# Kernel optimization log

Hardware: AMD Instinct MI355X
Metric: run time of the kernel (lower is better)

Reference implementation:

```python
import jax, jax.numpy as jnp
import numpy as np
import math

EMBED_DIM = 768
NUM_HEADS = 12
SEQ_LEN = 2048
NUM_BLOCKS = 8
BLOCK_SIZE = EMBED_DIM // NUM_BLOCKS  # 96
HEAD_DIM = EMBED_DIM // NUM_HEADS     # 64
BATCH = 4


def build_sparse_mask(T):
    # local window of 5 (j in [i-4, i]) plus log-stride links at i-8, i-16, ...
    m = np.full((T, T), -np.inf, dtype=np.float32)
    for i in range(T):
        for j in range(max(0, i - 4), i + 1):
            m[i, j] = 0.0
        step = 8
        while i - step >= 0:
            m[i, i - step] = 0.0
            step *= 2
    return jnp.asarray(m)


def make_urdhva_params(key):
    k1, k2, k3 = jax.random.split(key, 3)
    s = BLOCK_SIZE ** 0.5
    Wv = jax.random.normal(k1, (NUM_BLOCKS, BLOCK_SIZE, BLOCK_SIZE), jnp.float32) / s
    Wr = jax.random.normal(k2, (NUM_BLOCKS - 1, BLOCK_SIZE, BLOCK_SIZE), jnp.float32) / s
    Wl = jax.random.normal(k3, (NUM_BLOCKS - 1, BLOCK_SIZE, BLOCK_SIZE), jnp.float32) / s
    b = jnp.zeros((EMBED_DIM,), jnp.float32)
    return Wv, Wr, Wl, b


def urdhva_linear(x, Wv, Wr, Wl, b):
    # x: [..., EMBED_DIM] -> block-diagonal + neighbor cross-block linear
    shp = x.shape
    xb = x.reshape(-1, NUM_BLOCKS, BLOCK_SIZE)  # [N, B, S]
    y = jnp.einsum('nbs,bst->nbt', xb, Wv)
    y = y.at[:, 1:, :].add(jnp.einsum('nbs,bst->nbt', xb[:, :-1, :], Wr))
    y = y.at[:, :-1, :].add(jnp.einsum('nbs,bst->nbt', xb[:, 1:, :], Wl))
    return y.reshape(shp) + b


def setup_inputs() -> dict:
    key = jax.random.key(0)
    kx, kq, kk, kv, ko = jax.random.split(key, 5)
    inp = {'x': jax.random.normal(kx, (BATCH, SEQ_LEN, EMBED_DIM), jnp.float32)}
    for name, k in (('q', kq), ('k', kk), ('v', kv), ('o', ko)):
        Wv, Wr, Wl, b = make_urdhva_params(k)
        inp[name + '_Wv'] = Wv
        inp[name + '_Wr'] = Wr
        inp[name + '_Wl'] = Wl
        inp[name + '_b'] = b
    inp['sparse_mask'] = build_sparse_mask(SEQ_LEN)
    return inp


def reference(x, q_Wv, q_Wr, q_Wl, q_b, k_Wv, k_Wr, k_Wl, k_b,
              v_Wv, v_Wr, v_Wl, v_b, o_Wv, o_Wr, o_Wl, o_b, sparse_mask):
    B, T, C = x.shape
    H, D = NUM_HEADS, HEAD_DIM
    q = urdhva_linear(x, q_Wv, q_Wr, q_Wl, q_b).reshape(B, T, H, D).transpose(0, 2, 1, 3)
    k = urdhva_linear(x, k_Wv, k_Wr, k_Wl, k_b).reshape(B, T, H, D).transpose(0, 2, 1, 3)
    v = urdhva_linear(x, v_Wv, v_Wr, v_Wl, v_b).reshape(B, T, H, D).transpose(0, 2, 1, 3)
    scores = jnp.einsum('bhqd,bhkd->bhqk', q, k) / math.sqrt(D)
    scores = scores + sparse_mask[:T, :T]
    attn = jax.nn.softmax(scores, axis=-1)
    out = jnp.einsum('bhqk,bhkd->bhqd', attn, v).transpose(0, 2, 1, 3).reshape(B, T, C)
    return urdhva_linear(out, o_Wv, o_Wr, o_Wl, o_b)
```

## Files before the change

kernel.cpp:

```cpp
#include <hip/hip_runtime.h>
#include <hip/hip_bf16.h>

typedef __hip_bfloat16 bf16;
typedef __attribute__((ext_vector_type(8))) short short8;
typedef __attribute__((ext_vector_type(4))) float f32x4;

#define ED 768
#define NB 8
#define BS 96
#define NH 12
#define HD 64
#define SEQ 2048
#define NBATCH 4
#define NROWS (NBATCH*SEQ)

__device__ __forceinline__ float b2f(bf16 v){ return __bfloat162float(v); }
__device__ __forceinline__ bf16 f2b(float v){ return __float2bfloat16(v); }
__device__ __forceinline__ short f2bs(float v){
    return (short)__builtin_bit_cast(unsigned short, __float2bfloat16(v));
}
__device__ __forceinline__ unsigned pkbf16(float lo, float hi){
    return (unsigned)(unsigned short)f2bs(lo) |
           ((unsigned)(unsigned short)f2bs(hi) << 16);
}
__device__ __forceinline__ void gload_lds16(const void* g, void* l) {
    __builtin_amdgcn_global_load_lds(
        (const __attribute__((address_space(1))) unsigned*)g,
        (__attribute__((address_space(3))) unsigned*)l, 16, 0, 0);
}

__global__ __launch_bounds__(256) void densify_t(
    const float* __restrict__ qWv, const float* __restrict__ qWr, const float* __restrict__ qWl,
    const float* __restrict__ kWv, const float* __restrict__ kWr, const float* __restrict__ kWl,
    const float* __restrict__ vWv, const float* __restrict__ vWr, const float* __restrict__ vWl,
    const float* __restrict__ oWv, const float* __restrict__ oWr, const float* __restrict__ oWl,
    bf16* __restrict__ WdBase)
{
    __shared__ __align__(16) bf16 tile[96][104];

    const int z = blockIdx.y;
    const float* Wv = (z==0)?qWv:(z==1)?kWv:(z==2)?vWv:oWv;
    const float* Wr = (z==0)?qWr:(z==1)?kWr:(z==2)?vWr:oWr;
    const float* Wl = (z==0)?qWl:(z==1)?kWl:(z==2)?vWl:oWl;
    bf16* Wd = WdBase + (size_t)z*ED*ED;

    const int m = blockIdx.x;
    const float* src; int bt, bs;
    if (m < 8)       { src = Wv + m*96*96;      bt = m;    bs = m;    }
    else if (m < 15) { src = Wr + (m-8)*96*96;  bt = m-7;  bs = m-8;  }
    else             { src = Wl + (m-15)*96*96; bt = m-15; bs = m-14; }

    const int tid = threadIdx.x;
    for (int i = tid; i < 96*96; i += 256) {
        const int ss = i / 96, tt = i - ss*96;
        tile[tt][ss] = f2b(src[i]);
    }
    __syncthreads();
    for (int i = tid; i < 96*12; i += 256) {
        const int tt = i / 12, s8 = (i - tt*12) << 3;
        *(short8*)(Wd + (size_t)(bt*96+tt)*ED + bs*96 + s8) =
            *(const short8*)&tile[tt][s8];
    }
    if (m < 8) {
        const int lo   = (bt == 0) ? 0 : (bt-1)*96;
        const int hi0  = (bt >= 7) ? ED : (bt+2)*96;
        const int zlo8 = lo >> 3;
        const int ztot = zlo8 + ((ED - hi0) >> 3);
        const short8 zz = (short8){0,0,0,0,0,0,0,0};
        for (int i = tid; i < 96*ztot; i += 256) {
            const int tt = i / ztot, q = i - tt*ztot;
            const int col8 = (q < zlo8) ? (q << 3) : (hi0 + ((q - zlo8) << 3));
            *(short8*)(Wd + (size_t)(bt*96+tt)*ED + col8) = zz;
        }
    }
}

__global__ __launch_bounds__(256, 2) void qkv_gemm_fused(
    const float* __restrict__ x,
    const bf16* __restrict__ WdBase,
    const float* __restrict__ qb, const float* __restrict__ kb,
    const float* __restrict__ vb,
    bf16* __restrict__ qo, bf16* __restrict__ ko, bf16* __restrict__ vT)
{
    __shared__ __align__(16) bf16 As[2][128*32];
    __shared__ __align__(16) bf16 Bs[2][3*96*32];

    const int tid  = threadIdx.x;
    const int lane = tid & 63;
    const int wave = tid >> 6;
    const int rowbase = blockIdx.x*128;
    const int ob = blockIdx.y;
    const int colbase = ob*BS;
    const int klo = (ob==0)    ? 0  : (ob-1)*BS;
    const int khi = (ob==NB-1) ? ED : (ob+2)*BS;
    const int nt  = (khi - klo) >> 5;

    const int ar  = tid >> 1;
    const int ah  = tid & 1;
    const int asw = ((ar & 15) ^ ((ar & 15) >> 2)) & 3;
    const int as0 = ((2*ah)   ^ asw) << 4;
    const int as1 = ((2*ah+1) ^ asw) << 4;
    const float* axbase = x + (size_t)(rowbase + ar)*ED + 16*ah;

    const int sub  = lane >> 2;
    const int slot = lane & 3;
    const int sws  = (sub ^ (sub >> 2)) & 3;
    const int kofs = ((slot ^ sws) << 3);

    f32x4 acc[3][2][6];
    #pragma unroll
    for (int z=0;z<3;++z)
        #pragma unroll
        for (int i=0;i<2;++i)
            #pragma unroll
            for (int j=0;j<6;++j) acc[z][i][j] = (f32x4){0.f,0.f,0.f,0.f};

    float4 fr0, fr1, fr2, fr3;
    #define STAGE_A_LOAD(K0) do { \
        const float* ap = axbase + (K0); \
        fr0 = *(const float4*)ap; fr1 = *(const float4*)(ap+4); \
        fr2 = *(const float4*)(ap+8); fr3 = *(const float4*)(ap+12); } while(0)

    #define STAGE_A_WRITE(BUF) do { \
        short8 lo, hi; \
        lo[0]=f2bs(fr0.x); lo[1]=f2bs(fr0.y); lo[2]=f2bs(fr0.z); lo[3]=f2bs(fr0.w); \
        lo[4]=f2bs(fr1.x); lo[5]=f2bs(fr1.y); lo[6]=f2bs(fr1.z); lo[7]=f2bs(fr1.w); \
        hi[0]=f2bs(fr2.x); hi[1]=f2bs(fr2.y); hi[2]=f2bs(fr2.z); hi[3]=f2bs(fr2.w); \
        hi[4]=f2bs(fr3.x); hi[5]=f2bs(fr3.y); hi[6]=f2bs(fr3.z); hi[7]=f2bs(fr3.w); \
        char* abase = (char*)(BUF) + ar*64; \
        *(short8*)(abase + as0) = lo; \
        *(short8*)(abase + as1) = hi; } while(0)

    #define STAGE_B(K0, BUF) do { \
        _Pragma("unroll") \
        for (int zz = 0; zz < 3; ++zz) \
            for (int c = wave; c < 6; c += 4) { \
                const int r = c*16 + sub; \
                gload_lds16(WdBase + (size_t)zz*ED*ED + \
                            (size_t)(colbase + r)*ED + (K0) + kofs, \
                            (char*)(BUF) + zz*6144 + c*1024); \
            } } while(0)

    STAGE_A_LOAD(klo);
    STAGE_B(klo, Bs[0]);
    STAGE_A_WRITE(As[0]);
    __syncthreads();

    const int l15 = lane & 15;
    const int s   = lane >> 4;
    const int swr = (l15 ^ (l15 >> 2)) & 3;
    const int rsel = ((s ^ swr) << 4);

    #define COMPUTE(BUFA, BUFB) do { \
        short8 a0 = *(const short8*)((const char*)(BUFA) + (wave*32 + l15)*64 + rsel); \
        short8 a1 = *(const short8*)((const char*)(BUFA) + (wave*32 + 16 + l15)*64 + rsel); \
        _Pragma("unroll") \
        for (int zz = 0; zz < 3; ++zz) { \
            short8 b[6]; \
            _Pragma("unroll") \
            for (int nf = 0; nf < 6; ++nf) \
                b[nf] = *(const short8*)((const char*)(BUFB) + zz*6144 + \
                            (nf*16 + l15)*64 + rsel); \
            _Pragma("unroll") \
            for (int nf = 0; nf < 6; ++nf) { \
                acc[zz][0][nf] = __builtin_amdgcn_mfma_f32_16x16x32_bf16(a0, b[nf], acc[zz][0][nf], 0,0,0); \
                acc[zz][1][nf] = __builtin_amdgcn_mfma_f32_16x16x32_bf16(a1, b[nf], acc[zz][1][nf], 0,0,0); \
            } } } while(0)

    int cur = 0;
    for (int t = 0; t < nt-1; ++t) {
        STAGE_A_LOAD(klo + (t+1)*32);
        STAGE_B(klo + (t+1)*32, Bs[cur^1]);
        COMPUTE(As[cur], Bs[cur]);
        STAGE_A_WRITE(As[cur^1]);
        __syncthreads();
        cur ^= 1;
    }
    COMPUTE(As[cur], Bs[cur]);

    const int rbase = (lane >> 4) * 4;
    const int wrow = rowbase + wave*32;
    #pragma unroll
    for (int zz = 0; zz < 3; ++zz) {
        const float* bias = (zz==0) ? qb : (zz==1) ? kb : vb;
        #pragma unroll
        for (int rf = 0; rf < 2; ++rf) {
            #pragma unroll
            for (int nf = 0; nf < 6; ++nf) {
                const int col = colbase + nf*16 + l15;
                const float bv = bias[col];
                if (zz == 2) {
                    const int row0 = wrow + rf*16 + rbase;
                    uint2 dw;
                    dw.x = pkbf16(acc[2][rf][nf][0] + bv, acc[2][rf][nf][1] + bv);
                    dw.y = pkbf16(acc[2][rf][nf][2] + bv, acc[2][rf][nf][3] + bv);
                    *(uint2*)(vT + ((size_t)(row0 >> 4)*ED + col)*16 + (row0 & 15)) = dw;
                } else {
                    bf16* outp = (zz==0) ? qo : ko;
                    #pragma unroll
                    for (int r = 0; r < 4; ++r) {
                        const int row = wrow + rf*16 + rbase + r;
                        outp[(size_t)row*ED + col] = f2b(acc[zz][rf][nf][r] + bv);
                    }
                }
            }
        }
    }
    #undef STAGE_A_LOAD
    #undef STAGE_A_WRITE
    #undef STAGE_B
    #undef COMPUTE
}

__device__ __forceinline__ void stage64(
    const bf16* __restrict__ Ag, const bf16* __restrict__ Wd,
    int rowbase, int colbase, int k0,
    bf16* As, bf16* Bs, int wave, int lane)
{
    const int r8 = lane >> 3;
    const int sl = lane & 7;
    const int kofs = ((sl ^ r8) << 3);
    #pragma unroll
    for (int c = wave; c < 28; c += 4) {
        if (c < 16) {
            const int row = c*8 + r8;
            gload_lds16(Ag + (size_t)(rowbase + row)*ED + k0 + kofs,
                        (char*)As + c*1024);
        } else {
            const int row = (c-16)*8 + r8;
            gload_lds16(Wd + (size_t)(colbase + row)*ED + k0 + kofs,
                        (char*)Bs + (c-16)*1024);
        }
    }
}

__device__ __forceinline__ void compute64(
    const bf16* As, const bf16* Bs, int wave, int lane, f32x4 acc[2][6])
{
    const int l15 = lane & 15;
    const int s   = lane >> 4;
    #pragma unroll
    for (int ks = 0; ks < 2; ++ks) {
        short8 a[2], b[6];
        #pragma unroll
        for (int rf = 0; rf < 2; ++rf) {
            const int row = wave*32 + rf*16 + l15;
            a[rf] = *(const short8*)((const char*)As + row*128 +
                        ((((ks<<2)+s) ^ (row&7)) << 4));
        }
        #pragma unroll
        for (int nf = 0; nf < 6; ++nf) {
            const int row = nf*16 + l15;
            b[nf] = *(const short8*)((const char*)Bs + row*128 +
                        ((((ks<<2)+s) ^ (row&7)) << 4));
        }
        #pragma unroll
        for (int rf = 0; rf < 2; ++rf)
            #pragma unroll
            for (int nf = 0; nf < 6; ++nf)
                acc[rf][nf] = __builtin_amdgcn_mfma_f32_16x16x32_bf16(
                                  a[rf], b[nf], acc[rf][nf], 0, 0, 0);
    }
}

__device__ __forceinline__ void stage32o(
    const bf16* __restrict__ Ag, const bf16* __restrict__ Wd,
    int rowbase, int colbase, int k0,
    bf16* As, bf16* Bs, int wave, int lane)
{
    const int sub  = lane >> 2;
    const int slot = lane & 3;
    const int sws  = (sub ^ (sub >> 2)) & 3;
    const int kofs = ((slot ^ sws) << 3);
    #pragma unroll
    for (int c = wave; c < 14; c += 4) {
        if (c < 8) {
            const int r = c*16 + sub;
            gload_lds16(Ag + (size_t)(rowbase + r)*ED + k0 + kofs,
                        (char*)As + c*1024);
        } else {
            const int col = (c-8)*16 + sub;
            gload_lds16(Wd + (size_t)(colbase + col)*ED + k0 + kofs,
                        (char*)Bs + (c-8)*1024);
        }
    }
}

__device__ __forceinline__ void compute32o(
    const bf16* As, const bf16* Bs, int wave, int lane, f32x4 acc[2][6])
{
    const int l15 = lane & 15;
    const int s   = lane >> 4;
    const int swr = (l15 ^ (l15 >> 2)) & 3;
    const int rsel = ((s ^ swr) << 4);

    short8 a[2], b[6];
    #pragma unroll
    for (int rf = 0; rf < 2; ++rf)
        a[rf] = *(const short8*)((const char*)As +
                    (wave*32 + rf*16 + l15)*64 + rsel);
    #pragma unroll
    for (int nf = 0; nf < 6; ++nf)
        b[nf] = *(const short8*)((const char*)Bs + (nf*16 + l15)*64 + rsel);
    #pragma unroll
    for (int rf = 0; rf < 2; ++rf)
        #pragma unroll
        for (int nf = 0; nf < 6; ++nf)
            acc[rf][nf] = __builtin_amdgcn_mfma_f32_16x16x32_bf16(
                              a[rf], b[nf], acc[rf][nf], 0, 0, 0);
}

__global__ __launch_bounds__(256, 2) void o_gemm_lds(
    const bf16* __restrict__ A,
    const bf16* __restrict__ Wd,
    const float* __restrict__ bias,
    float* __restrict__ Out)
{
    __shared__ __align__(16) bf16 As[2][128*64];
    __shared__ __align__(16) bf16 Bs[2][96*64];

    const int lane = threadIdx.x & 63;
    const int wave = threadIdx.x >> 6;
    const int rowbase = blockIdx.x*128;
    const int ob = blockIdx.y;
    const int colbase = ob*BS;
    const int klo = (ob==0)    ? 0  : (ob-1)*BS;
    const int khi = (ob==NB-1) ? ED : (ob+2)*BS;
    const int band = khi - klo;
    const int nt64 = band >> 6;
    const bool tail = (band & 63) != 0;

    f32x4 acc[2][6];
    #pragma unroll
    for (int i=0;i<2;++i)
        #pragma unroll
        for (int j=0;j<6;++j) acc[i][j] = (f32x4){0.f,0.f,0.f,0.f};

    stage64(A, Wd, rowbase, colbase, klo, As[0], Bs[0], wave, lane);
    __syncthreads();
    int cur = 0;
    for (int t = 1; t < nt64; ++t) {
        stage64(A, Wd, rowbase, colbase, klo + t*64,
                As[cur^1], Bs[cur^1], wave, lane);
        compute64(As[cur], Bs[cur], wave, lane, acc);
        __syncthreads();
        cur ^= 1;
    }
    if (tail) {
        stage32o(A, Wd, rowbase, colbase, klo + nt64*64,
                 As[cur^1], Bs[cur^1], wave, lane);
        compute64(As[cur], Bs[cur], wave, lane, acc);
        __syncthreads();
        cur ^= 1;
        compute32o(As[cur], Bs[cur], wave, lane, acc);
    } else {
        compute64(As[cur], Bs[cur], wave, lane, acc);
    }

    const int l15 = lane & 15;
    const int rbase = (lane >> 4) * 4;
    const int wrow = rowbase + wave*32;
    #pragma unroll
    for (int rf = 0; rf < 2; ++rf) {
        #pragma unroll
        for (int nf = 0; nf < 6; ++nf) {
            const int col = colbase + nf*16 + l15;
            const float bv = bias[col];
            #pragma unroll
            for (int r = 0; r < 4; ++r) {
                const int row = wrow + rf*16 + rbase + r;
                Out[(size_t)row*ED + col] = acc[rf][nf][r] + bv;
            }
        }
    }
}

__global__ __launch_bounds__(256) void sparse_attn_mfma(
    const bf16* __restrict__ q, const bf16* __restrict__ k,
    const bf16* __restrict__ vT, bf16* __restrict__ out)
{
    __shared__ __align__(16) char shm[24*16*128];

    const int lane = threadIdx.x & 63;
    const int wid  = threadIdx.x >> 6;
    const int o   = (blockIdx.x & 7)*192 + (blockIdx.x >> 3);
    const int hb  = o >> 5;
    const int qt0 = (o & 31) << 2;
    const int h   = hb % NH;
    const int bb  = hb / NH;
    const int I   = qt0 << 4;
    const int i0  = I + (wid << 4);

    const int l15 = lane & 15;
    const int g   = lane >> 4;

    const bf16* qbase = q + ((size_t)bb*SEQ + i0 + l15)*ED + h*HD + g*8;
    const short8 qf0 = *(const short8*)qbase;
    const short8 qf1 = *(const short8*)(qbase + 32);

    int bases[8];
    bases[0]=i0;     bases[1]=i0-16;  bases[2]=i0-32;  bases[3]=i0-64;
    bases[4]=i0-128; bases[5]=i0-256; bases[6]=i0-512; bases[7]=i0-1024;

    short8 vfrag[4][4];
    #pragma unroll
    for (int u = 0; u < 4; ++u) {
        const int tb = (g & 2) ? bases[2*u+1] : bases[2*u];
        const size_t gt = (size_t)bb*128 + ((tb < 0 ? 0 : tb) >> 4);
        #pragma unroll
        for (int nt = 0; nt < 4; ++nt)
            vfrag[u][nt] = *(const short8*)(vT +
                (gt*ED + h*HD + 16*nt + l15)*16 + 8*(g & 1));
    }

    const bf16* kbb = k + (size_t)bb*SEQ*ED + h*HD;
    #pragma unroll
    for (int c = 0; c < 12; ++c) {
        const int id  = c*256 + threadIdx.x;
        const int row = id >> 3;
        const int sl  = id & 7;
        const int j   = row >> 4;
        int tb;
        if (j < 8) tb = I + 48 - (j << 4);
        else       tb = I + (((j-8) >> 2) << 4) - (128 << ((j-8) & 3));
        const int gr = (tb < 0 ? 0 : tb) + (row & 15);
        gload_lds16(kbb + (size_t)gr*ED + ((sl ^ (row & 7)) << 3),
                    shm + id*16);
    }
    __syncthreads();

    float p[8][4];
    #pragma unroll
    for (int t = 0; t < 8; ++t) {
        const int j = (t < 4) ? ((t == 3 ? 7 : 3 + t) - wid)
                              : (8 + 4*wid + (t - 4));
        f32x4 acc = (f32x4){0.f,0.f,0.f,0.f};
        if (bases[t] >= 0) {
            const char* kr = shm + (j*16 + l15)*128;
            const int sw = l15 & 7;
            const short8 kf0 = *(const short8*)(kr + ((g ^ sw) << 4));
            const short8 kf1 = *(const short8*)(kr + (((g+4) ^ sw) << 4));
            acc = __builtin_amdgcn_mfma_f32_16x16x32_bf16(kf0, qf0, acc, 0,0,0);
            acc = __builtin_amdgcn_mfma_f32_16x16x32_bf16(kf1, qf1, acc, 0,0,0);
        }
        const int Dt = i0 - bases[t];
        #pragma unroll
        for (int r = 0; r < 4; ++r) {
            const int delta = Dt + l15 - 4*g - r;
            const bool val = (bases[t] >= 0) &&
                (((unsigned)delta <= 4u) ||
                 (delta >= 8 && (delta & (delta-1)) == 0));
            p[t][r] = val ? acc[r]*0.125f : -1e30f;
        }
    }

    float m = -1e30f;
    #pragma unroll
    for (int t = 0; t < 8; ++t)
        #pragma unroll
        for (int r = 0; r < 4; ++r) m = fmaxf(m, p[t][r]);
    m = fmaxf(m, __shfl_xor(m, 16));
    m = fmaxf(m, __shfl_xor(m, 32));

    float den = 0.f;
    #pragma unroll
    for (int t = 0; t < 8; ++t)
        #pragma unroll
        for (int r = 0; r < 4; ++r) { p[t][r] = __expf(p[t][r] - m); den += p[t][r]; }
    den += __shfl_xor(den, 16);
    den += __shfl_xor(den, 32);
    const float inv = 1.f / den;

    __syncthreads();

    {
        char* prow = shm + wid*4352 + l15*272;
        #pragma unroll
        for (int t = 0; t < 8; ++t) {
            *(unsigned*)(prow + 32*t + 8*g)     = pkbf16(p[t][0]*inv, p[t][1]*inv);
            *(unsigned*)(prow + 32*t + 8*g + 4) = pkbf16(p[t][2]*inv, p[t][3]*inv);
        }
    }

    f32x4 accO[4];
    #pragma unroll
    for (int nt = 0; nt < 4; ++nt) accO[nt] = (f32x4){0.f,0.f,0.f,0.f};

    #pragma unroll
    for (int u = 0; u < 4; ++u) {
        const short8 pa = *(const short8*)(shm + wid*4352 + l15*272 + 64*u + 16*g);
        #pragma unroll
        for (int nt = 0; nt < 4; ++nt)
            accO[nt] = __builtin_amdgcn_mfma_f32_16x16x32_bf16(
                           pa, vfrag[u][nt], accO[nt], 0,0,0);
    }

    #pragma unroll
    for (int nt = 0; nt < 4; ++nt)
        #pragma unroll
        for (int r = 0; r < 4; ++r)
            out[((size_t)bb*SEQ + i0 + 4*g + r)*ED + h*HD + 16*nt + l15] =
                f2b(accO[nt][r]);
}

extern "C" void kernel_launch(void* const* d_in, const int* in_sizes, int n_in,
                              void* d_out, int out_size, void* d_ws, size_t ws_size,
                              hipStream_t stream) {
    const float* x   = (const float*)d_in[0];
    const float* qWv = (const float*)d_in[1];
    const float* qWr = (const float*)d_in[2];
    const float* qWl = (const float*)d_in[3];
    const float* qb  = (const float*)d_in[4];
    const float* kWv = (const float*)d_in[5];
    const float* kWr = (const float*)d_in[6];
    const float* kWl = (const float*)d_in[7];
    const float* kb  = (const float*)d_in[8];
    const float* vWv = (const float*)d_in[9];
    const float* vWr = (const float*)d_in[10];
    const float* vWl = (const float*)d_in[11];
    const float* vb  = (const float*)d_in[12];
    const float* oWv = (const float*)d_in[13];
    const float* oWr = (const float*)d_in[14];
    const float* oWl = (const float*)d_in[15];
    const float* ob  = (const float*)d_in[16];

    const size_t QKV = (size_t)NROWS*ED;
    bf16* q   = (bf16*)d_ws;
    bf16* k   = q + QKV;
    bf16* vT  = k + QKV;
    bf16* ao  = vT + QKV;
    bf16* Wd  = ao + QKV;
    bf16* Wdo = Wd + (size_t)3*ED*ED;

    densify_t<<<dim3(22, 4), 256, 0, stream>>>(
        qWv,qWr,qWl, kWv,kWr,kWl, vWv,vWr,vWl, oWv,oWr,oWl, Wd);

    qkv_gemm_fused<<<dim3(NROWS/128, NB), 256, 0, stream>>>(
        x, Wd, qb, kb, vb, q, k, vT);

    sparse_attn_mfma<<<(NBATCH*NH*(SEQ/16))/4, 256, 0, stream>>>(q, k, vT, ao);

    o_gemm_lds<<<dim3(NROWS/128, NB), 256, 0, stream>>>(ao, Wdo, ob, (float*)d_out);
}
```

Baseline: 63.24 us.

## Triple-buffer B tiles in QKV GEMM with counted vmcnt barriers

The QKV GEMM now keeps three shared-memory buffers for the weight tiles and prefetches B two k-steps ahead, while A stays double-buffered. The full __syncthreads is replaced by an explicit s_waitcnt with a per-wave vmcnt count, so the newest direct-to-LDS loads can stay in flight across the barrier. This is meant to hide global load latency better, at the cost of more LDS per block, which may reduce occupancy. The hand-tuned vmcnt counts must match the number of loads each wave issues, so correctness depends on that bookkeeping.

```diff
diff --git a/kernel.cpp b/kernel.cpp
--- a/kernel.cpp
+++ b/kernel.cpp
@@ -83,7 +83,7 @@
     bf16* __restrict__ qo, bf16* __restrict__ ko, bf16* __restrict__ vT)
 {
     __shared__ __align__(16) bf16 As[2][128*32];
-    __shared__ __align__(16) bf16 Bs[2][3*96*32];
+    __shared__ __align__(16) bf16 Bs[3][3*96*32];
 
     const int tid  = threadIdx.x;
     const int lane = tid & 63;
@@ -141,10 +141,22 @@
                             (char*)(BUF) + zz*6144 + c*1024); \
             } } while(0)
 
+    #define PIPE_BARRIER_COUNTED() do { \
+        if (wave < 2) asm volatile("s_waitcnt vmcnt(6) lgkmcnt(0)" ::: "memory"); \
+        else          asm volatile("s_waitcnt vmcnt(3) lgkmcnt(0)" ::: "memory"); \
+        __builtin_amdgcn_s_barrier(); \
+        __builtin_amdgcn_sched_barrier(0); } while(0)
+
+    #define PIPE_BARRIER_DRAIN() do { \
+        asm volatile("s_waitcnt vmcnt(0) lgkmcnt(0)" ::: "memory"); \
+        __builtin_amdgcn_s_barrier(); \
+        __builtin_amdgcn_sched_barrier(0); } while(0)
+
     STAGE_A_LOAD(klo);
+    STAGE_A_WRITE(As[0]);
     STAGE_B(klo, Bs[0]);
-    STAGE_A_WRITE(As[0]);
-    __syncthreads();
+    STAGE_B(klo + 32, Bs[1]);
+    PIPE_BARRIER_COUNTED();
 
     const int l15 = lane & 15;
     const int s   = lane >> 4;
@@ -167,16 +179,22 @@
                 acc[zz][1][nf] = __builtin_amdgcn_mfma_f32_16x16x32_bf16(a1, b[nf], acc[zz][1][nf], 0,0,0); \
             } } } while(0)
 
-    int cur = 0;
+    int acur = 0, bcur = 0;
     for (int t = 0; t < nt-1; ++t) {
         STAGE_A_LOAD(klo + (t+1)*32);
-        STAGE_B(klo + (t+1)*32, Bs[cur^1]);
-        COMPUTE(As[cur], Bs[cur]);
-        STAGE_A_WRITE(As[cur^1]);
-        __syncthreads();
-        cur ^= 1;
-    }
-    COMPUTE(As[cur], Bs[cur]);
+        const bool more = (t + 2 < nt);
+        if (more) {
+            int b2 = bcur + 2; if (b2 >= 3) b2 -= 3;
+            STAGE_B(klo + (t+2)*32, Bs[b2]);
+        }
+        COMPUTE(As[acur], Bs[bcur]);
+        STAGE_A_WRITE(As[acur^1]);
+        if (more) PIPE_BARRIER_COUNTED();
+        else      PIPE_BARRIER_DRAIN();
+        acur ^= 1;
+        if (++bcur == 3) bcur = 0;
+    }
+    COMPUTE(As[acur], Bs[bcur]);
 
     const int rbase = (lane >> 4) * 4;
     const int wrow = rowbase + wave*32;
@@ -210,6 +228,8 @@
     #undef STAGE_A_WRITE
     #undef STAGE_B
     #undef COMPUTE
+    #undef PIPE_BARRIER_COUNTED
+    #undef PIPE_BARRIER_DRAIN
 }
 
 __device__ __forceinline__ void stage64(
```

Result: no change. 63.26 us (+0.0%).
